# Kernel tuning notes

Measured on AMD Instinct MI355X. Metric: run time of the kernel, lower is better.

## Reference

```python
import jax, jax.numpy as jnp
import numpy as np

IN_DIM = 64
OUT_DIM = 16  # SPD matrix side
HIDDEN = [128, 128]
CHOL_DIM = OUT_DIM + OUT_DIM * (OUT_DIM - 1) // 2  # 136
BATCH = 65536
LEAKY_SLOPE = 0.01  # torch.nn.LeakyReLU default


def _uniform(key, shape, in_feat):
    b = 1.0 / in_feat
    return jax.random.uniform(key, shape, jnp.float32, -b, b)


def setup_inputs() -> dict:
    key = jax.random.key(0)
    ks = jax.random.split(key, 7)
    x = jax.random.normal(ks[0], (BATCH, IN_DIM), jnp.float32)
    # layer sizes: 64 -> 128 -> 128 -> 136, init uniform(-1/in_feat, 1/in_feat)
    W1 = _uniform(ks[1], (IN_DIM, HIDDEN[0]), IN_DIM)
    b1 = _uniform(ks[2], (HIDDEN[0],), IN_DIM)
    W2 = _uniform(ks[3], (HIDDEN[0], HIDDEN[1]), HIDDEN[0])
    b2 = _uniform(ks[4], (HIDDEN[1],), HIDDEN[0])
    W3 = _uniform(ks[5], (HIDDEN[1], CHOL_DIM), HIDDEN[1])
    b3 = _uniform(ks[6], (CHOL_DIM,), HIDDEN[1])
    return {"x": x, "W1": W1, "b1": b1, "W2": W2, "b2": b2, "W3": W3, "b3": b3}


def reference(x, W1, b1, W2, b2, W3, b3):
    # MLP with LeakyReLU between layers, then Tanh on final output
    h = jax.nn.leaky_relu(x @ W1 + b1, LEAKY_SLOPE)
    h = jax.nn.leaky_relu(h @ W2 + b2, LEAKY_SLOPE)
    ldata = jnp.tanh(h @ W3 + b3)  # [B, 136]

    # fill_tril: scatter the 136 values into the lower triangle (row-major)
    rows, cols = jnp.tril_indices(OUT_DIM)
    L = jnp.zeros((x.shape[0], OUT_DIM, OUT_DIM), x.dtype).at[:, rows, cols].set(ldata)
    Q = L + jnp.swapaxes(L, -1, -2)  # symmetric [B, 16, 16]

    # symmetric eigendecomposition (ascending eigenvalues, like torch.symeig)
    w, V = jnp.linalg.eigh(Q)
    # sqrt(softmax(exp(w)**2)) ; exp(w)**2 == exp(2w)
    ev = jnp.sqrt(jax.nn.softmax(jnp.exp(2.0 * w), axis=-1))  # [B, 16]
    # faithful to source: uses inverse (== V^T in exact math since V orthogonal)
    Vinv = jnp.linalg.inv(V)
    # V @ diag(ev) @ V^{-1}
    return jnp.einsum('bij,bj,bjk->bik', V, ev, Vinv)
```

## Files before the change

kernel.cpp:

```cpp
#include <hip/hip_runtime.h>
#include <math.h>

typedef _Float16 f16;
typedef _Float16 half4_t __attribute__((ext_vector_type(4)));
typedef _Float16 half8_t __attribute__((ext_vector_type(8)));
typedef float floatx4 __attribute__((ext_vector_type(4)));

__global__ __launch_bounds__(256) void prep_weights(
    const float* __restrict__ W1, const float* __restrict__ W2,
    const float* __restrict__ W3, f16* __restrict__ wt) {
  int t = blockIdx.x * 256 + threadIdx.x;
  if (t < 8192) {
    int c = t >> 6, k = t & 63;
    wt[t] = (f16)W1[k * 128 + c];
  } else if (t < 24576) {
    int u = t - 8192;
    int c = u >> 7, k = u & 127;
    wt[t] = (f16)W2[k * 128 + c];
  } else if (t < 43008) {
    int u = t - 24576;
    int c = u >> 7, k = u & 127;
    wt[t] = (f16)((c < 136) ? W3[k * 136 + c] : 0.0f);
  }
}

__device__ __forceinline__ float fast_tanh(float v) {
  float e = __builtin_amdgcn_exp2f(v * 2.885390081777926814f);
  return 1.0f - 2.0f * __builtin_amdgcn_rcpf(e + 1.0f);
}

template <int CTRL>
__device__ __forceinline__ float dpp_add(float v) {
  int t = __builtin_amdgcn_update_dpp(0, __builtin_bit_cast(int, v), CTRL,
                                      0xf, 0xf, true);
  return v + __builtin_bit_cast(float, t);
}
__device__ __forceinline__ float wsum(float v) {
  v = dpp_add<0x111>(v);
  v = dpp_add<0x112>(v);
  v = dpp_add<0x114>(v);
  v = dpp_add<0x118>(v);
  v = dpp_add<0x142>(v);
  v = dpp_add<0x143>(v);
  return __builtin_bit_cast(
      float, __builtin_amdgcn_readlane(__builtin_bit_cast(int, v), 63));
}

__device__ __forceinline__ half4_t to_h(floatx4 v) {
  auto p0 = __builtin_amdgcn_cvt_pkrtz(v[0], v[1]);
  auto p1 = __builtin_amdgcn_cvt_pkrtz(v[2], v[3]);
  half4_t h;
  h[0] = p0[0]; h[1] = p0[1]; h[2] = p1[0]; h[3] = p1[1];
  return h;
}

__device__ __forceinline__ floatx4 expm_c(floatx4 b, floatx4 I4, float& m) {
  float s2 = wsum(b[0] * b[0] + b[1] * b[1] + b[2] * b[2] + b[3] * b[3]);
  float td = wsum(I4[0] * b[0] + I4[1] * b[1] + I4[2] * b[2] + I4[3] * b[3]);
  m = td * 0.0625f;
  float fr2 = fmaxf(s2 - td * m, 1e-30f);
  int e2 = (int)(__builtin_bit_cast(unsigned, fr2) >> 23) - 127;
  int s = (e2 + 5) >> 1;
  s = s < 0 ? 0 : (s > 12 ? 12 : s);
  s = __builtin_amdgcn_readfirstlane(s);
  float sc = __builtin_bit_cast(float, (unsigned)(127 - s) << 23);
  b = (b - I4 * m) * sc;
  half4_t bh = to_h(b);
  floatx4 zero = {0.f, 0.f, 0.f, 0.f};
  floatx4 a2 = __builtin_amdgcn_mfma_f32_16x16x16f16(bh, bh, zero, 0, 0, 0);
  floatx4 t = I4 * 0.5f + b * (1.f / 6.f) + a2 * (1.f / 24.f);
  floatx4 p = __builtin_amdgcn_mfma_f32_16x16x16f16(to_h(a2), to_h(t), I4 + b,
                                                    0, 0, 0);
  for (int k = 0; k < s; ++k) {
    half4_t ph = to_h(p);
    p = __builtin_amdgcn_mfma_f32_16x16x16f16(ph, ph, zero, 0, 0, 0);
  }
  return p;
}

__global__ __launch_bounds__(256, 2) void fused_kernel(
    const float* __restrict__ x, const float* __restrict__ b1,
    const float* __restrict__ b2v, const float* __restrict__ b3,
    const f16* __restrict__ wt, float* __restrict__ out) {
  __shared__ f16 act1[2048];
  __shared__ f16 act2[2048];
  __shared__ f16 lds_ld[32 * 144];

  const int lane = threadIdx.x & 63;
  const int w = threadIdx.x >> 6;
  const int cl = lane & 15;
  const int q = lane >> 4;
  const f16* w1t = wt;
  const f16* w2t = wt + 8192;
  const f16* w3t = wt + 24576;

  half8_t w1f[2][2], w2f[2][4], w3f[3][4];
  float bias1[2], bias2[2], bias3[3];
#pragma unroll
  for (int j = 0; j < 2; ++j) {
    int c8g = w + 4 * j;
    int c = c8g * 16 + cl;
#pragma unroll
    for (int ks = 0; ks < 2; ++ks)
      w1f[j][ks] = *(const half8_t*)(w1t + c * 64 + ks * 32 + q * 8);
#pragma unroll
    for (int ks = 0; ks < 4; ++ks)
      w2f[j][ks] = *(const half8_t*)(w2t + c * 128 + ks * 32 + q * 8);
    bias1[j] = b1[c];
    bias2[j] = b2v[c];
  }
#pragma unroll
  for (int j = 0; j < 3; ++j) {
    int c8g = w + 4 * j;
    int c8c = c8g < 9 ? c8g : 8;
    int c = c8c * 16 + cl;
#pragma unroll
    for (int ks = 0; ks < 4; ++ks)
      w3f[j][ks] = *(const half8_t*)(w3t + c * 128 + ks * 32 + q * 8);
    int cc = c8g * 16 + cl;
    bias3[j] = (cc < 136) ? b3[cc] : 0.f;
  }

  const int r0b = blockIdx.x * 32;
  const float* xp = x + (size_t)(r0b + cl) * 64 + q * 8;
  floatx4 v0 = *(const floatx4*)xp;
  floatx4 v1 = *(const floatx4*)(xp + 4);
  floatx4 v2 = *(const floatx4*)(xp + 32);
  floatx4 v3 = *(const floatx4*)(xp + 36);

  for (int t = 0; t < 2; ++t) {
    half8_t a0, a1;
#pragma unroll
    for (int i = 0; i < 4; ++i) {
      a0[i] = (f16)v0[i]; a0[i + 4] = (f16)v1[i];
      a1[i] = (f16)v2[i]; a1[i + 4] = (f16)v3[i];
    }
    if (t == 0) {
      xp = x + (size_t)(r0b + 16 + cl) * 64 + q * 8;
      v0 = *(const floatx4*)xp;
      v1 = *(const floatx4*)(xp + 4);
      v2 = *(const floatx4*)(xp + 32);
      v3 = *(const floatx4*)(xp + 36);
    }

#pragma unroll
    for (int j = 0; j < 2; ++j) {
      int c8g = w + 4 * j;
      floatx4 acc = {0.f, 0.f, 0.f, 0.f};
      acc = __builtin_amdgcn_mfma_f32_16x16x32_f16(a0, w1f[j][0], acc, 0, 0, 0);
      acc = __builtin_amdgcn_mfma_f32_16x16x32_f16(a1, w1f[j][1], acc, 0, 0, 0);
#pragma unroll
      for (int i = 0; i < 4; ++i) {
        float v = acc[i] + bias1[j];
        v = v > 0.f ? v : 0.01f * v;
        int row = q * 4 + i;
        int gs = ((c8g * 2 + (cl >> 3)) ^ row) & 15;
        act1[row * 128 + gs * 8 + (cl & 7)] = (f16)v;
      }
    }
    __syncthreads();

    half8_t ha[4];
#pragma unroll
    for (int ks = 0; ks < 4; ++ks)
      ha[ks] = *(const half8_t*)(act1 + cl * 128 +
                                 ((((ks << 2) | q) ^ cl) << 3));

#pragma unroll
    for (int j = 0; j < 2; ++j) {
      int c8g = w + 4 * j;
      floatx4 acc = {0.f, 0.f, 0.f, 0.f};
#pragma unroll
      for (int ks = 0; ks < 4; ++ks)
        acc = __builtin_amdgcn_mfma_f32_16x16x32_f16(ha[ks], w2f[j][ks], acc,
                                                     0, 0, 0);
#pragma unroll
      for (int i = 0; i < 4; ++i) {
        float v = acc[i] + bias2[j];
        v = v > 0.f ? v : 0.01f * v;
        int row = q * 4 + i;
        int gs = ((c8g * 2 + (cl >> 3)) ^ row) & 15;
        act2[row * 128 + gs * 8 + (cl & 7)] = (f16)v;
      }
    }
    __syncthreads();

#pragma unroll
    for (int ks = 0; ks < 4; ++ks)
      ha[ks] = *(const half8_t*)(act2 + cl * 128 +
                                 ((((ks << 2) | q) ^ cl) << 3));

#pragma unroll
    for (int j = 0; j < 3; ++j) {
      int c8g = w + 4 * j;
      if (c8g < 9) {
        floatx4 acc = {0.f, 0.f, 0.f, 0.f};
#pragma unroll
        for (int ks = 0; ks < 4; ++ks)
          acc = __builtin_amdgcn_mfma_f32_16x16x32_f16(ha[ks], w3f[j][ks], acc,
                                                       0, 0, 0);
        int c = c8g * 16 + cl;
#pragma unroll
        for (int i = 0; i < 4; ++i) {
          float v = fast_tanh(acc[i] + bias3[j]);
          lds_ld[(t * 16 + q * 4 + i) * 144 + c] = (f16)v;
        }
      }
    }
  }
  __syncthreads();

  const int r = cl;
#pragma unroll 2
  for (int jj = 0; jj < 8; ++jj) {
    int m_loc = w * 8 + jj;
    const f16* ld = lds_ld + m_loc * 144;

    floatx4 b, I4;
#pragma unroll
    for (int i = 0; i < 4; ++i) {
      int k = q * 4 + i;
      int hi = r > k ? r : k;
      int lo = r + k - hi;
      float v = (float)ld[hi * (hi + 1) / 2 + lo];
      bool d = (r == k);
      I4[i] = d ? 1.f : 0.f;
      b[i] = d ? 4.f * v : 2.f * v;
    }

    float m1;
    floatx4 p = expm_c(b, I4, m1);
    float fac = __builtin_amdgcn_exp2f(m1 * 1.4426950408889634f - 1.0f);
    float m2;
    p = expm_c(p * fac, I4, m2);

    float n2 = wsum(p[0] * p[0] + p[1] * p[1] + p[2] * p[2] + p[3] * p[3]);
    float inv = __builtin_amdgcn_rsqf(n2);
    floatx4 o = p * inv;
    size_t mat = (size_t)(r0b + m_loc);
    *(floatx4*)(out + mat * 256 + r * 16 + q * 4) = o;
  }
}

extern "C" void kernel_launch(void* const* d_in, const int* in_sizes, int n_in,
                              void* d_out, int out_size, void* d_ws,
                              size_t ws_size, hipStream_t stream) {
  const float* x = (const float*)d_in[0];
  const float* W1 = (const float*)d_in[1];
  const float* b1 = (const float*)d_in[2];
  const float* W2 = (const float*)d_in[3];
  const float* b2 = (const float*)d_in[4];
  const float* W3 = (const float*)d_in[5];
  const float* b3 = (const float*)d_in[6];
  float* out = (float*)d_out;
  f16* wt = (f16*)d_ws;

  prep_weights<<<168, 256, 0, stream>>>(W1, W2, W3, wt);
  fused_kernel<<<2048, 256, 0, stream>>>(x, b1, b2, b3, wt, out);
}
```

Measured before the change: 130.9 us.

## Split fused MLP and matrix-exponential kernel into two separate kernels

Unfuses the kernel: an MLP kernel writes the tanh outputs as f16 to a workspace buffer, and a separate expm kernel reads them back with one matrix per wavefront. The aim is to let each stage run at its own occupancy (launch bounds 4 for the MLP, an unconstrained one-matrix-per-wave expm), so the register-heavy expm no longer limits the MLP. In exchange it adds a global round-trip of about 17 MB and an extra kernel launch, and the expm stage now launches 16384 blocks.

Measured after the change: 176.4 us. 34.8% more time.

```diff
diff --git a/kernel.cpp b/kernel.cpp
--- a/kernel.cpp
+++ b/kernel.cpp
@@ -5,6 +5,8 @@
 typedef _Float16 half4_t __attribute__((ext_vector_type(4)));
 typedef _Float16 half8_t __attribute__((ext_vector_type(8)));
 typedef float floatx4 __attribute__((ext_vector_type(4)));
+
+#define LDATA_OFF_BYTES 86016
 
 __global__ __launch_bounds__(256) void prep_weights(
     const float* __restrict__ W1, const float* __restrict__ W2,
@@ -27,6 +29,139 @@
 __device__ __forceinline__ float fast_tanh(float v) {
   float e = __builtin_amdgcn_exp2f(v * 2.885390081777926814f);
   return 1.0f - 2.0f * __builtin_amdgcn_rcpf(e + 1.0f);
+}
+
+__global__ __launch_bounds__(256, 4) void mlp_kernel(
+    const float* __restrict__ x, const float* __restrict__ b1,
+    const float* __restrict__ b2v, const float* __restrict__ b3,
+    const f16* __restrict__ wt, f16* __restrict__ ldata) {
+  __shared__ f16 act1[2048];
+  __shared__ f16 act2[2048];
+
+  const int lane = threadIdx.x & 63;
+  const int w = threadIdx.x >> 6;
+  const int cl = lane & 15;
+  const int q = lane >> 4;
+  const f16* w1t = wt;
+  const f16* w2t = wt + 8192;
+  const f16* w3t = wt + 24576;
+
+  half8_t w1f[2][2], w2f[2][4], w3f[3][4];
+  float bias1[2], bias2[2], bias3[3];
+#pragma unroll
+  for (int j = 0; j < 2; ++j) {
+    int c8g = w + 4 * j;
+    int c = c8g * 16 + cl;
+#pragma unroll
+    for (int ks = 0; ks < 2; ++ks)
+      w1f[j][ks] = *(const half8_t*)(w1t + c * 64 + ks * 32 + q * 8);
+#pragma unroll
+    for (int ks = 0; ks < 4; ++ks)
+      w2f[j][ks] = *(const half8_t*)(w2t + c * 128 + ks * 32 + q * 8);
+    bias1[j] = b1[c];
+    bias2[j] = b2v[c];
+  }
+#pragma unroll
+  for (int j = 0; j < 3; ++j) {
+    int c8g = w + 4 * j;
+    int c8c = c8g < 9 ? c8g : 8;
+    int c = c8c * 16 + cl;
+#pragma unroll
+    for (int ks = 0; ks < 4; ++ks)
+      w3f[j][ks] = *(const half8_t*)(w3t + c * 128 + ks * 32 + q * 8);
+    int cc = c8g * 16 + cl;
+    bias3[j] = (cc < 136) ? b3[cc] : 0.f;
+  }
+
+  const int r0b = blockIdx.x * 32;
+  const float* xp = x + (size_t)(r0b + cl) * 64 + q * 8;
+  floatx4 v0 = *(const floatx4*)xp;
+  floatx4 v1 = *(const floatx4*)(xp + 4);
+  floatx4 v2 = *(const floatx4*)(xp + 32);
+  floatx4 v3 = *(const floatx4*)(xp + 36);
+
+  for (int t = 0; t < 2; ++t) {
+    half8_t a0, a1;
+#pragma unroll
+    for (int i = 0; i < 4; ++i) {
+      a0[i] = (f16)v0[i]; a0[i + 4] = (f16)v1[i];
+      a1[i] = (f16)v2[i]; a1[i + 4] = (f16)v3[i];
+    }
+    if (t == 0) {
+      xp = x + (size_t)(r0b + 16 + cl) * 64 + q * 8;
+      v0 = *(const floatx4*)xp;
+      v1 = *(const floatx4*)(xp + 4);
+      v2 = *(const floatx4*)(xp + 32);
+      v3 = *(const floatx4*)(xp + 36);
+    }
+
+#pragma unroll
+    for (int j = 0; j < 2; ++j) {
+      int c8g = w + 4 * j;
+      floatx4 acc = {0.f, 0.f, 0.f, 0.f};
+      acc = __builtin_amdgcn_mfma_f32_16x16x32_f16(a0, w1f[j][0], acc, 0, 0, 0);
+      acc = __builtin_amdgcn_mfma_f32_16x16x32_f16(a1, w1f[j][1], acc, 0, 0, 0);
+#pragma unroll
+      for (int i = 0; i < 4; ++i) {
+        float v = acc[i] + bias1[j];
+        v = v > 0.f ? v : 0.01f * v;
+        int row = q * 4 + i;
+        int gs = ((c8g * 2 + (cl >> 3)) ^ row) & 15;
+        act1[row * 128 + gs * 8 + (cl & 7)] = (f16)v;
+      }
+    }
+    __syncthreads();
+
+    half8_t ha[4];
+#pragma unroll
+    for (int ks = 0; ks < 4; ++ks)
+      ha[ks] = *(const half8_t*)(act1 + cl * 128 +
+                                 ((((ks << 2) | q) ^ cl) << 3));
+
+#pragma unroll
+    for (int j = 0; j < 2; ++j) {
+      int c8g = w + 4 * j;
+      floatx4 acc = {0.f, 0.f, 0.f, 0.f};
+#pragma unroll
+      for (int ks = 0; ks < 4; ++ks)
+        acc = __builtin_amdgcn_mfma_f32_16x16x32_f16(ha[ks], w2f[j][ks], acc,
+                                                     0, 0, 0);
+#pragma unroll
+      for (int i = 0; i < 4; ++i) {
+        float v = acc[i] + bias2[j];
+        v = v > 0.f ? v : 0.01f * v;
+        int row = q * 4 + i;
+        int gs = ((c8g * 2 + (cl >> 3)) ^ row) & 15;
+        act2[row * 128 + gs * 8 + (cl & 7)] = (f16)v;
+      }
+    }
+    __syncthreads();
+
+#pragma unroll
+    for (int ks = 0; ks < 4; ++ks)
+      ha[ks] = *(const half8_t*)(act2 + cl * 128 +
+                                 ((((ks << 2) | q) ^ cl) << 3));
+
+#pragma unroll
+    for (int j = 0; j < 3; ++j) {
+      int c8g = w + 4 * j;
+      if (c8g < 9) {
+        floatx4 acc = {0.f, 0.f, 0.f, 0.f};
+#pragma unroll
+        for (int ks = 0; ks < 4; ++ks)
+          acc = __builtin_amdgcn_mfma_f32_16x16x32_f16(ha[ks], w3f[j][ks], acc,
+                                                       0, 0, 0);
+        int c = c8g * 16 + cl;
+        if (c < 136) {
+#pragma unroll
+          for (int i = 0; i < 4; ++i) {
+            int r = r0b + t * 16 + q * 4 + i;
+            ldata[(size_t)r * 136 + c] = (f16)fast_tanh(acc[i] + bias3[j]);
+          }
+        }
+      }
+    }
+  }
 }
 
 template <int CTRL>
@@ -78,168 +213,35 @@
   return p;
 }
 
-__global__ __launch_bounds__(256, 2) void fused_kernel(
-    const float* __restrict__ x, const float* __restrict__ b1,
-    const float* __restrict__ b2v, const float* __restrict__ b3,
-    const f16* __restrict__ wt, float* __restrict__ out) {
-  __shared__ f16 act1[2048];
-  __shared__ f16 act2[2048];
-  __shared__ f16 lds_ld[32 * 144];
-
+__global__ __launch_bounds__(256) void expm_kernel(
+    const f16* __restrict__ ldata, float* __restrict__ out) {
   const int lane = threadIdx.x & 63;
-  const int w = threadIdx.x >> 6;
-  const int cl = lane & 15;
-  const int q = lane >> 4;
-  const f16* w1t = wt;
-  const f16* w2t = wt + 8192;
-  const f16* w3t = wt + 24576;
-
-  half8_t w1f[2][2], w2f[2][4], w3f[3][4];
-  float bias1[2], bias2[2], bias3[3];
-#pragma unroll
-  for (int j = 0; j < 2; ++j) {
-    int c8g = w + 4 * j;
-    int c = c8g * 16 + cl;
-#pragma unroll
-    for (int ks = 0; ks < 2; ++ks)
-      w1f[j][ks] = *(const half8_t*)(w1t + c * 64 + ks * 32 + q * 8);
-#pragma unroll
-    for (int ks = 0; ks < 4; ++ks)
-      w2f[j][ks] = *(const half8_t*)(w2t + c * 128 + ks * 32 + q * 8);
-    bias1[j] = b1[c];
-    bias2[j] = b2v[c];
-  }
-#pragma unroll
-  for (int j = 0; j < 3; ++j) {
-    int c8g = w + 4 * j;
-    int c8c = c8g < 9 ? c8g : 8;
-    int c = c8c * 16 + cl;
-#pragma unroll
-    for (int ks = 0; ks < 4; ++ks)
-      w3f[j][ks] = *(const half8_t*)(w3t + c * 128 + ks * 32 + q * 8);
-    int cc = c8g * 16 + cl;
-    bias3[j] = (cc < 136) ? b3[cc] : 0.f;
-  }
-
-  const int r0b = blockIdx.x * 32;
-  const float* xp = x + (size_t)(r0b + cl) * 64 + q * 8;
-  floatx4 v0 = *(const floatx4*)xp;
-  floatx4 v1 = *(const floatx4*)(xp + 4);
-  floatx4 v2 = *(const floatx4*)(xp + 32);
-  floatx4 v3 = *(const floatx4*)(xp + 36);
-
-  for (int t = 0; t < 2; ++t) {
-    half8_t a0, a1;
-#pragma unroll
-    for (int i = 0; i < 4; ++i) {
-      a0[i] = (f16)v0[i]; a0[i + 4] = (f16)v1[i];
-      a1[i] = (f16)v2[i]; a1[i + 4] = (f16)v3[i];
-    }
-    if (t == 0) {
-      xp = x + (size_t)(r0b + 16 + cl) * 64 + q * 8;
-      v0 = *(const floatx4*)xp;
-      v1 = *(const floatx4*)(xp + 4);
-      v2 = *(const floatx4*)(xp + 32);
-      v3 = *(const floatx4*)(xp + 36);
-    }
-
-#pragma unroll
-    for (int j = 0; j < 2; ++j) {
-      int c8g = w + 4 * j;
-      floatx4 acc = {0.f, 0.f, 0.f, 0.f};
-      acc = __builtin_amdgcn_mfma_f32_16x16x32_f16(a0, w1f[j][0], acc, 0, 0, 0);
-      acc = __builtin_amdgcn_mfma_f32_16x16x32_f16(a1, w1f[j][1], acc, 0, 0, 0);
-#pragma unroll
-      for (int i = 0; i < 4; ++i) {
-        float v = acc[i] + bias1[j];
-        v = v > 0.f ? v : 0.01f * v;
-        int row = q * 4 + i;
-        int gs = ((c8g * 2 + (cl >> 3)) ^ row) & 15;
-        act1[row * 128 + gs * 8 + (cl & 7)] = (f16)v;
-      }
-    }
-    __syncthreads();
-
-    half8_t ha[4];
-#pragma unroll
-    for (int ks = 0; ks < 4; ++ks)
-      ha[ks] = *(const half8_t*)(act1 + cl * 128 +
-                                 ((((ks << 2) | q) ^ cl) << 3));
-
-#pragma unroll
-    for (int j = 0; j < 2; ++j) {
-      int c8g = w + 4 * j;
-      floatx4 acc = {0.f, 0.f, 0.f, 0.f};
-#pragma unroll
-      for (int ks = 0; ks < 4; ++ks)
-        acc = __builtin_amdgcn_mfma_f32_16x16x32_f16(ha[ks], w2f[j][ks], acc,
-                                                     0, 0, 0);
-#pragma unroll
-      for (int i = 0; i < 4; ++i) {
-        float v = acc[i] + bias2[j];
-        v = v > 0.f ? v : 0.01f * v;
-        int row = q * 4 + i;
-        int gs = ((c8g * 2 + (cl >> 3)) ^ row) & 15;
-        act2[row * 128 + gs * 8 + (cl & 7)] = (f16)v;
-      }
-    }
-    __syncthreads();
-
-#pragma unroll
-    for (int ks = 0; ks < 4; ++ks)
-      ha[ks] = *(const half8_t*)(act2 + cl * 128 +
-                                 ((((ks << 2) | q) ^ cl) << 3));
-
-#pragma unroll
-    for (int j = 0; j < 3; ++j) {
-      int c8g = w + 4 * j;
-      if (c8g < 9) {
-        floatx4 acc = {0.f, 0.f, 0.f, 0.f};
-#pragma unroll
-        for (int ks = 0; ks < 4; ++ks)
-          acc = __builtin_amdgcn_mfma_f32_16x16x32_f16(ha[ks], w3f[j][ks], acc,
-                                                       0, 0, 0);
-        int c = c8g * 16 + cl;
-#pragma unroll
-        for (int i = 0; i < 4; ++i) {
-          float v = fast_tanh(acc[i] + bias3[j]);
-          lds_ld[(t * 16 + q * 4 + i) * 144 + c] = (f16)v;
-        }
-      }
-    }
-  }
-  __syncthreads();
-
-  const int r = cl;
-#pragma unroll 2
-  for (int jj = 0; jj < 8; ++jj) {
-    int m_loc = w * 8 + jj;
-    const f16* ld = lds_ld + m_loc * 144;
-
-    floatx4 b, I4;
-#pragma unroll
-    for (int i = 0; i < 4; ++i) {
-      int k = q * 4 + i;
-      int hi = r > k ? r : k;
-      int lo = r + k - hi;
-      float v = (float)ld[hi * (hi + 1) / 2 + lo];
-      bool d = (r == k);
-      I4[i] = d ? 1.f : 0.f;
-      b[i] = d ? 4.f * v : 2.f * v;
-    }
-
-    float m1;
-    floatx4 p = expm_c(b, I4, m1);
-    float fac = __builtin_amdgcn_exp2f(m1 * 1.4426950408889634f - 1.0f);
-    float m2;
-    p = expm_c(p * fac, I4, m2);
-
-    float n2 = wsum(p[0] * p[0] + p[1] * p[1] + p[2] * p[2] + p[3] * p[3]);
-    float inv = __builtin_amdgcn_rsqf(n2);
-    floatx4 o = p * inv;
-    size_t mat = (size_t)(r0b + m_loc);
-    *(floatx4*)(out + mat * 256 + r * 16 + q * 4) = o;
-  }
+  const int mat = (int)((blockIdx.x * 256u + threadIdx.x) >> 6);
+  const int r = lane & 15, q = lane >> 4;
+  const f16* ld = ldata + (size_t)mat * 136;
+
+  floatx4 b, I4;
+#pragma unroll
+  for (int i = 0; i < 4; ++i) {
+    int k = q * 4 + i;
+    int hi = r > k ? r : k;
+    int lo = r + k - hi;
+    float v = (float)ld[hi * (hi + 1) / 2 + lo];
+    bool d = (r == k);
+    I4[i] = d ? 1.f : 0.f;
+    b[i] = d ? 4.f * v : 2.f * v;
+  }
+
+  float m1;
+  floatx4 p = expm_c(b, I4, m1);
+  float fac = __builtin_amdgcn_exp2f(m1 * 1.4426950408889634f - 1.0f);
+  float m2;
+  p = expm_c(p * fac, I4, m2);
+
+  float n2 = wsum(p[0] * p[0] + p[1] * p[1] + p[2] * p[2] + p[3] * p[3]);
+  float inv = __builtin_amdgcn_rsqf(n2);
+  floatx4 o = p * inv;
+  *(floatx4*)(out + (size_t)mat * 256 + r * 16 + q * 4) = o;
 }
 
 extern "C" void kernel_launch(void* const* d_in, const int* in_sizes, int n_in,
@@ -254,7 +256,9 @@
   const float* b3 = (const float*)d_in[6];
   float* out = (float*)d_out;
   f16* wt = (f16*)d_ws;
+  f16* ldata = (f16*)((char*)d_ws + LDATA_OFF_BYTES);
 
   prep_weights<<<168, 256, 0, stream>>>(W1, W2, W3, wt);
-  fused_kernel<<<2048, 256, 0, stream>>>(x, b1, b2, b3, wt, out);
-}
+  mlp_kernel<<<2048, 256, 0, stream>>>(x, b1, b2, b3, wt, ldata);
+  expm_kernel<<<16384, 256, 0, stream>>>(ldata, out);
+}
```
